# Performance work log

Measured on AMD Instinct MI355X. Metric: run time of the kernel, lower is better.

The kernel has to match this reference:

```python
import jax, jax.numpy as jnp
import numpy as np

SOFTCAP = 50.0
EPS = 1e-6
N_HEADS, D_HEAD = 16, 64


def _rms(x, w):
    return x * jax.lax.rsqrt(jnp.mean(x * x, axis=-1, keepdims=True) + EPS) * w


def _rope(x, cos, sin):
    # Faithful to source: apply_rope uses x.size(1) as the position axis, but is
    # called on (B, H, T, Dh) tensors, so positions are indexed by HEAD index.
    n = x.shape[1]
    x1, x2 = x[..., 0::2], x[..., 1::2]
    c = cos[:n][None, :, None, :]
    s = sin[:n][None, :, None, :]
    return jnp.stack([x1 * c - x2 * s, x1 * s + x2 * c], axis=-1).reshape(x.shape)


def setup_inputs() -> dict:
    key = jax.random.key(0)
    ks = jax.random.split(key, 12)
    L, D, H, Dh, Dff, V, B, T = 6, 1024, N_HEADS, D_HEAD, 4096, 32000, 1, 1024
    r = lambda k, shape: jax.random.normal(k, shape, dtype=jnp.float32) * 0.02
    return {
        'x': jax.random.randint(ks[0], (B, T), 0, V, dtype=jnp.int32),
        'embed': r(ks[1], (V, D)),
        'ln1': jnp.ones((L, D), jnp.float32),
        'Wq': r(ks[2], (L, H * Dh, D)),
        'Wk': r(ks[3], (L, H * Dh, D)),
        'Wv': r(ks[4], (L, H * Dh, D)),
        'Wo': r(ks[5], (L, D, H * Dh)),
        'qn': jnp.ones((L, Dh), jnp.float32),
        'kn': jnp.ones((L, Dh), jnp.float32),
        'ln2': jnp.ones((L, D), jnp.float32),
        'Wg': r(ks[6], (L, Dff, D)),
        'Wu': r(ks[7], (L, Dff, D)),
        'Wd': r(ks[8], (L, D, Dff)),
        'ln_out': jnp.ones((D,), jnp.float32),
    }


def reference(x, embed, ln1, Wq, Wk, Wv, Wo, qn, kn, ln2, Wg, Wu, Wd, ln_out):
    B, T = x.shape
    H, Dh = N_HEADS, D_HEAD
    scale = Dh ** -0.5
    # RoPE tables (theta=10000)
    freqs = 1.0 / (10000.0 ** (jnp.arange(0, Dh, 2, dtype=jnp.float32) / Dh))
    ang = jnp.arange(T, dtype=jnp.float32)[:, None] * freqs[None, :]
    cos, sin = jnp.cos(ang), jnp.sin(ang)
    mask = jnp.triu(jnp.ones((T, T), dtype=bool), k=1)  # True above diagonal

    h = embed[x]  # (B, T, D)

    def block(h, p):
        l1, wq, wk, wv, wo, qnw, knw, l2, wg, wu, wd = p
        hn = _rms(h, l1)
        q = (hn @ wq.T).reshape(B, T, H, Dh).transpose(0, 2, 1, 3)  # (B,H,T,Dh)
        k = (hn @ wk.T).reshape(B, T, H, Dh).transpose(0, 2, 1, 3)
        v = (hn @ wv.T).reshape(B, T, H, Dh).transpose(0, 2, 1, 3)
        q = _rope(_rms(q, qnw), cos, sin)
        k = _rope(_rms(k, knw), cos, sin)
        scores = jnp.einsum('bhtd,bhsd->bhts', q, k) * scale
        scores = SOFTCAP * jnp.tanh(scores / SOFTCAP)
        scores = jnp.where(mask[None, None], -jnp.inf, scores)
        attn = jax.nn.softmax(scores, axis=-1)
        o = jnp.einsum('bhts,bhsd->bhtd', attn, v)
        o = o.transpose(0, 2, 1, 3).reshape(B, T, H * Dh)
        h = h + o @ wo.T
        hn2 = _rms(h, l2)
        h = h + (jax.nn.silu(hn2 @ wg.T) * (hn2 @ wu.T)) @ wd.T
        return h, None

    h, _ = jax.lax.scan(block, h, (ln1, Wq, Wk, Wv, Wo, qn, kn, ln2, Wg, Wu, Wd))
    # tied embed/head
    logits = _rms(h, ln_out) @ embed.T  # (B, T, V)
    return logits
```

## Files before the change

kernel.cpp:

```cpp
#include <hip/hip_runtime.h>
#include <math.h>
#include <type_traits>

typedef __bf16 bf16_t;
typedef bf16_t bf16x4 __attribute__((ext_vector_type(4)));
typedef bf16_t bf16x8 __attribute__((ext_vector_type(8)));
typedef float  f32x4  __attribute__((ext_vector_type(4)));

#define RMS_EPS 1e-6f

enum { EP_STORE = 0, EP_RESID = 1, EP_SPLIT = 2, EP_SILU = 3, EP_QKV = 4 };

template<int V> using IC = std::integral_constant<int, V>;

static __device__ __forceinline__ f32x4 mfma16(bf16x8 a, bf16x8 b, f32x4 c) {
    return __builtin_amdgcn_mfma_f32_16x16x32_bf16(a, b, c, 0, 0, 0);
}

#define GLDS(gp, lp) __builtin_amdgcn_global_load_lds( \
    (const __attribute__((address_space(1))) void*)(gp), \
    (__attribute__((address_space(3))) void*)(lp), 16, 0, 0)

template<int N> static __device__ __forceinline__ void vmwait() {
    if constexpr (N == 0)      asm volatile("s_waitcnt vmcnt(0)" ::: "memory");
    else if constexpr (N == 2) asm volatile("s_waitcnt vmcnt(2)" ::: "memory");
    else if constexpr (N == 3) asm volatile("s_waitcnt vmcnt(3)" ::: "memory");
    else if constexpr (N == 4) asm volatile("s_waitcnt vmcnt(4)" ::: "memory");
    else if constexpr (N == 6) asm volatile("s_waitcnt vmcnt(6)" ::: "memory");
    else if constexpr (N == 8) asm volatile("s_waitcnt vmcnt(8)" ::: "memory");
    __builtin_amdgcn_sched_barrier(0);
}
static __device__ __forceinline__ void bar() { __builtin_amdgcn_s_barrier(); }

template<int BM, int BN, int WR, int WC, int PLANES, int EPIL, int MINW>
__global__ __launch_bounds__(WR * WC * 64, MINW)
void gemm_bf16(const bf16_t* __restrict__ Ah, const bf16_t* __restrict__ Al,
               const bf16_t* __restrict__ Bh,
               float* __restrict__ Cf, bf16_t* __restrict__ Ch, bf16_t* __restrict__ Cl,
               int K, int lda, int ldb, int ldc, long long sC,
               const float* __restrict__ qnw, const float* __restrict__ knw)
{
    constexpr int ASZ = BM * 32, BSZ = BN * 32;
    constexpr int NW = WR * WC;
    constexpr int NLD = (BM / 16 * (PLANES >= 2 ? 2 : 1) + BN / 16) / NW;
    __shared__ __align__(16) bf16_t sAh[2][ASZ], sBh[2][BSZ];
    __shared__ __align__(16) bf16_t sAl[PLANES >= 2 ? 2 : 1][PLANES >= 2 ? ASZ : 8];

    const int gx = gridDim.x;
    int id = blockIdx.x + gx * blockIdx.y;
    if (gridDim.z == 1) {
        int nwg = gx * gridDim.y;
        int q = nwg >> 3, r = nwg & 7;
        int xcd = id & 7, ix = id >> 3;
        id = (xcd < r ? xcd * (q + 1) : r * (q + 1) + (xcd - r) * q) + ix;
    }
    const int bm = id % gx, bn = id / gx;
    const int row0 = bm * BM, col0 = bn * BN;

    const size_t kofs = (size_t)blockIdx.z * K;
    Ah += kofs;  Bh += kofs;
    if constexpr (PLANES >= 2) Al += kofs;

    const int tid = threadIdx.x, lane = tid & 63, wave = tid >> 6;
    const int lr = lane & 15, lg = lane >> 4;
    constexpr int WM = BM / WR, WN = BN / WC, MF = WM / 16, NF = WN / 16;
    const int wr = wave / WC, wc = wave % WC;

    f32x4 acc[MF][NF];
    #pragma unroll
    for (int m = 0; m < MF; ++m)
        #pragma unroll
        for (int n = 0; n < NF; ++n) acc[m][n] = (f32x4){0.f, 0.f, 0.f, 0.f};

    auto stage = [&](int k0, auto pc) {
        constexpr int p = decltype(pc)::value;
        #pragma unroll
        for (int i = wave; i < BM / 16; i += NW) {
            int s = i * 64 + lane, rr = s >> 2, c = s & 3;
            size_t go = (size_t)(row0 + rr) * lda + k0 + ((c ^ ((rr >> 1) & 3)) << 3);
            GLDS(Ah + go, &sAh[p][i * 512]);
            if constexpr (PLANES >= 2) GLDS(Al + go, &sAl[p][i * 512]);
        }
        #pragma unroll
        for (int i = wave; i < BN / 16; i += NW) {
            int s = i * 64 + lane, rr = s >> 2, c = s & 3;
            size_t go = (size_t)(col0 + rr) * ldb + k0 + ((c ^ ((rr >> 1) & 3)) << 3);
            GLDS(Bh + go, &sBh[p][i * 512]);
        }
    };

    auto compute = [&](auto pc) {
        constexpr int p = decltype(pc)::value;
        bf16x8 ahf[MF], alf[MF], bhf[NF];
        #pragma unroll
        for (int m = 0; m < MF; ++m) {
            int rr = wr * WM + m * 16 + lr;
            int by = rr * 64 + ((lg ^ ((rr >> 1) & 3)) << 4);
            ahf[m] = *(const bf16x8*)((const char*)&sAh[p][0] + by);
            if constexpr (PLANES >= 2)
                alf[m] = *(const bf16x8*)((const char*)&sAl[p][0] + by);
        }
        #pragma unroll
        for (int n = 0; n < NF; ++n) {
            int rr = wc * WN + n * 16 + lr;
            int by = rr * 64 + ((lg ^ ((rr >> 1) & 3)) << 4);
            bhf[n] = *(const bf16x8*)((const char*)&sBh[p][0] + by);
        }
        #pragma unroll
        for (int m = 0; m < MF; ++m)
            #pragma unroll
            for (int n = 0; n < NF; ++n) {
                acc[m][n] = mfma16(ahf[m], bhf[n], acc[m][n]);
                if constexpr (PLANES >= 2)
                    acc[m][n] = mfma16(alf[m], bhf[n], acc[m][n]);
            }
    };

    stage(0, IC<0>{});
    int k0 = 32;
    for (; k0 + 32 < K; k0 += 64) {
        stage(k0, IC<1>{});
        vmwait<NLD>(); bar();
        compute(IC<0>{});
        bar();
        stage(k0 + 32, IC<0>{});
        vmwait<NLD>(); bar();
        compute(IC<1>{});
        bar();
    }
    stage(k0, IC<1>{});
    vmwait<NLD>(); bar();
    compute(IC<0>{});
    bar();
    vmwait<0>(); bar();
    compute(IC<1>{});

    if constexpr (EPIL == EP_QKV) {
        const int colbase = col0 + wc * WN;
        const int typ = colbase >> 10;
        const float* nw = (typ == 0) ? qnw : knw;
        const int hh = (colbase - typ * 1024) >> 6;
        constexpr float kLogF = -0.41524101186092029f;
        #pragma unroll
        for (int m = 0; m < MF; ++m)
            #pragma unroll
            for (int r = 0; r < 4; ++r) {
                int grow = row0 + wr * WM + m * 16 + lg * 4 + r;
                if (typ < 2) {
                    float ss = 0.f;
                    #pragma unroll
                    for (int n = 0; n < NF; ++n) {
                        float v = acc[m][n][r];
                        ss += v * v;
                    }
                    ss += __shfl_xor(ss, 1, 64);
                    ss += __shfl_xor(ss, 2, 64);
                    ss += __shfl_xor(ss, 4, 64);
                    ss += __shfl_xor(ss, 8, 64);
                    float inv = rsqrtf(ss * (1.0f / 64.0f) + RMS_EPS);
                    #pragma unroll
                    for (int n = 0; n < NF; ++n) {
                        int i = n * 16 + lr;
                        float x = acc[m][n][r] * inv * nw[i];
                        float p = __shfl_xor(x, 1, 64);
                        float f = exp2f((float)(i >> 1) * kLogF);
                        float ang = (float)hh * f;
                        float cs = cosf(ang), sn = sinf(ang);
                        float o = (lr & 1) ? (p * sn + x * cs) : (x * cs - p * sn);
                        Ch[(size_t)grow * ldc + colbase + i] = (bf16_t)o;
                    }
                } else {
                    #pragma unroll
                    for (int n = 0; n < NF; ++n) {
                        float v = acc[m][n][r];
                        size_t off = (size_t)grow * ldc + colbase + n * 16 + lr;
                        bf16_t hb = (bf16_t)v;
                        Ch[off] = hb;
                        Cl[off] = (bf16_t)(v - (float)hb);
                    }
                }
            }
        return;
    }

    #pragma unroll
    for (int m = 0; m < MF; ++m)
        #pragma unroll
        for (int n = 0; n < NF; ++n)
            #pragma unroll
            for (int r = 0; r < 4; ++r) {
                int grow = row0 + wr * WM + m * 16 + lg * 4 + r;
                int gcol = col0 + wc * WN + n * 16 + lr;
                float v = acc[m][n][r];
                if constexpr (EPIL == EP_SILU) {
                    float pv = __shfl_xor(v, 1, 64);
                    if (!(lr & 1)) {
                        float s = (v / (1.0f + expf(-v))) * pv;
                        size_t off = (size_t)grow * ldc + (gcol >> 1);
                        Ch[off] = (bf16_t)s;
                    }
                } else {
                    size_t off = (size_t)blockIdx.z * sC + (size_t)grow * ldc + gcol;
                    if constexpr (EPIL == EP_STORE) {
                        Cf[off] = v;
                    } else if constexpr (EPIL == EP_RESID) {
                        Cf[off] += v;
                    } else {
                        bf16_t hb = (bf16_t)v;
                        Ch[off] = hb;
                        Cl[off] = (bf16_t)(v - (float)hb);
                    }
                }
            }
}

static __device__ __forceinline__ void wsplit_body(
    int b2, int tid,
    const float* wq, const float* wk, const float* wv, const float* wo,
    const float* wg, const float* wu, const float* wd,
    bf16_t* wAh, bf16_t* wGUh, bf16_t* wdh)
{
    #pragma unroll
    for (int k = 0; k < 4; ++k) {
        int b = b2 * 4 + k;
        const float* src;
        bf16_t* dst;
        size_t so, doff;
        if (b < 4096) {
            src = b < 1024 ? wq : b < 2048 ? wk : b < 3072 ? wv : wo;
            so = (size_t)(b & 1023) * 256 + tid;
            doff = (size_t)b * 256 + tid;
            dst = wAh;
        } else if (b < 12288) {
            int bb = b - 4096;
            int row = bb < 4096 ? 2 * bb : 2 * (bb - 4096) + 1;
            src = bb < 4096 ? wg : wu;
            so = (size_t)(bb & 4095) * 256 + tid;
            doff = (size_t)row * 256 + tid;
            dst = wGUh;
        } else {
            src = wd;
            so = (size_t)(b - 12288) * 256 + tid;
            doff = so;
            dst = wdh;
        }
        f32x4 v = ((const f32x4*)src)[so];
        bf16x4 hv;
        #pragma unroll
        for (int j = 0; j < 4; ++j) hv[j] = (bf16_t)v[j];
        ((bf16x4*)dst)[doff] = hv;
    }
}

__global__ __launch_bounds__(256)
void reduce_rms_wsplit(const float* __restrict__ p, float* __restrict__ h,
                       const float* __restrict__ w, bf16_t* __restrict__ outh,
                       const float* wq, const float* wk, const float* wv,
                       const float* wo, const float* wg, const float* wu,
                       const float* wd, bf16_t* wAh, bf16_t* wGUh, bf16_t* wdh)
{
    int blk = blockIdx.x, tid = threadIdx.x;
    if (blk >= 1024) {
        if (wq) wsplit_body(blk - 1024, tid, wq, wk, wv, wo, wg, wu, wd,
                            wAh, wGUh, wdh);
        return;
    }
    size_t i = (size_t)blk * 256 + tid;
    const size_t S = (1024 * 1024) / 4;
    f32x4 a = ((const f32x4*)p)[i];
    f32x4 b = ((const f32x4*)p)[i + S];
    f32x4 c = ((const f32x4*)p)[i + 2 * S];
    f32x4 d = ((const f32x4*)p)[i + 3 * S];
    f32x4 hv = ((const f32x4*)h)[i];
    #pragma unroll
    for (int j = 0; j < 4; ++j) hv[j] += (a[j] + b[j]) + (c[j] + d[j]);
    ((f32x4*)h)[i] = hv;

    float ss = hv[0]*hv[0] + hv[1]*hv[1] + hv[2]*hv[2] + hv[3]*hv[3];
    #pragma unroll
    for (int m = 1; m < 64; m <<= 1) ss += __shfl_xor(ss, m, 64);
    __shared__ float red[4];
    if ((tid & 63) == 0) red[tid >> 6] = ss;
    __syncthreads();
    float tot = red[0] + red[1] + red[2] + red[3];
    float inv = rsqrtf(tot * (1.0f / 1024.0f) + RMS_EPS);
    f32x4 wt4 = *(const f32x4*)(w + tid * 4);
    bf16x4 hv4;
    #pragma unroll
    for (int j = 0; j < 4; ++j) hv4[j] = (bf16_t)(hv[j] * inv * wt4[j]);
    ((bf16x4*)outh)[i] = hv4;
}

__global__ __launch_bounds__(256)
void gather_rms_wsplit(const int* __restrict__ ids, const float* __restrict__ embed,
                       const float* __restrict__ w, float* __restrict__ h,
                       bf16_t* __restrict__ outh,
                       const float* wq, const float* wk, const float* wv,
                       const float* wo, const float* wg, const float* wu,
                       const float* wd, bf16_t* wAh, bf16_t* wGUh, bf16_t* wdh)
{
    int blk = blockIdx.x, tid = threadIdx.x;
    if (blk >= 1024) {
        wsplit_body(blk - 1024, tid, wq, wk, wv, wo, wg, wu, wd, wAh, wGUh, wdh);
        return;
    }
    int row = ids[blk];
    f32x4 v = ((const f32x4*)(embed + (size_t)row * 1024))[tid];
    ((f32x4*)(h + (size_t)blk * 1024))[tid] = v;

    float ss = v[0]*v[0] + v[1]*v[1] + v[2]*v[2] + v[3]*v[3];
    #pragma unroll
    for (int m = 1; m < 64; m <<= 1) ss += __shfl_xor(ss, m, 64);
    __shared__ float red[4];
    if ((tid & 63) == 0) red[tid >> 6] = ss;
    __syncthreads();
    float tot = red[0] + red[1] + red[2] + red[3];
    float inv = rsqrtf(tot * (1.0f / 1024.0f) + RMS_EPS);
    f32x4 wt4 = *(const f32x4*)(w + tid * 4);
    bf16x4 hv;
    #pragma unroll
    for (int j = 0; j < 4; ++j) hv[j] = (bf16_t)(v[j] * inv * wt4[j]);
    ((bf16x4*)outh)[(size_t)blk * 256 + tid] = hv;
}

__global__ __launch_bounds__(128, 2)
void flash_attn(const bf16_t* __restrict__ qkvh,
                const bf16_t* __restrict__ vTh, const bf16_t* __restrict__ vTl,
                bf16_t* __restrict__ oh)
{
    __shared__ __align__(16) bf16_t sQ[32*64], sK[64*64], sVh[64*64], sVl[64*64];
    __shared__ __align__(16) bf16_t sPh[32*64], sPl[32*64];

    const int q0 = blockIdx.x * 32;
    const int hh = blockIdx.y;
    const int tid = threadIdx.x, lane = tid & 63, w = tid >> 6;
    const int lr = lane & 15, lg = lane >> 4;

    #pragma unroll
    for (int ii = 0; ii < 2; ++ii) {
        int r0 = w * 16 + ii * 8;
        int r  = r0 + (lane >> 3);
        int i  = lane & 7;
        GLDS(qkvh + (size_t)(q0 + r) * 3072 + hh * 64 + ((i ^ (r & 7)) << 3),
             sQ + r0 * 64);
    }
    __syncthreads();

    bf16x8 qa[2];
    #pragma unroll
    for (int ks = 0; ks < 2; ++ks) {
        int r = w * 16 + lr;
        qa[ks] = *(const bf16x8*)((const char*)sQ + r * 128 +
                                  ((((ks << 2) | lg) ^ (r & 7)) << 4));
    }

    f32x4 o_acc[4];
    #pragma unroll
    for (int n = 0; n < 4; ++n) o_acc[n] = (f32x4){0.f, 0.f, 0.f, 0.f};
    float m_run[4] = {-1e30f, -1e30f, -1e30f, -1e30f};
    float l_run[4] = {0.f, 0.f, 0.f, 0.f};

    const int ntiles = ((q0 + 31) >> 6) + 1;
    for (int t = 0; t < ntiles; ++t) {
        const int kv0 = t * 64;
        #pragma unroll
        for (int ii = 0; ii < 4; ++ii) {
            int r0 = w * 32 + ii * 8;
            int r  = r0 + (lane >> 3);
            int i  = lane & 7;
            GLDS(qkvh + (size_t)(kv0 + r) * 3072 + 1024 + hh * 64 + ((i ^ (r & 7)) << 3),
                 sK + r0 * 64);
            GLDS(vTh + (size_t)(hh * 64 + r) * 1024 + kv0 + ((i ^ (r & 7)) << 3),
                 sVh + r0 * 64);
            GLDS(vTl + (size_t)(hh * 64 + r) * 1024 + kv0 + ((i ^ (r & 7)) << 3),
                 sVl + r0 * 64);
        }
        __syncthreads();

        f32x4 s_acc[4];
        #pragma unroll
        for (int n = 0; n < 4; ++n) s_acc[n] = (f32x4){0.f, 0.f, 0.f, 0.f};
        #pragma unroll
        for (int ks = 0; ks < 2; ++ks)
            #pragma unroll
            for (int n = 0; n < 4; ++n) {
                int r = n * 16 + lr;
                bf16x8 kb = *(const bf16x8*)((const char*)sK + r * 128 +
                                             ((((ks << 2) | lg) ^ (r & 7)) << 4));
                s_acc[n] = mfma16(qa[ks], kb, s_acc[n]);
            }

        #pragma unroll
        for (int j = 0; j < 4; ++j) {
            int qr = q0 + w * 16 + lg * 4 + j;
            float p[4];
            float mx = -1e30f;
            #pragma unroll
            for (int n = 0; n < 4; ++n) {
                float v = s_acc[n][j] * 0.125f;
                v = 50.f * tanhf(v * 0.02f);
                int key = kv0 + n * 16 + lr;
                if (key > qr) v = -1e30f;
                p[n] = v;
                mx = fmaxf(mx, v);
            }
            #pragma unroll
            for (int m = 1; m < 16; m <<= 1) mx = fmaxf(mx, __shfl_xor(mx, m, 64));
            float mn = fmaxf(m_run[j], mx);
            float ef = __expf(m_run[j] - mn);
            m_run[j] = mn;
            float rs = 0.f;
            #pragma unroll
            for (int n = 0; n < 4; ++n) {
                float e = expf(p[n] - mn);
                p[n] = e;
                rs += e;
            }
            #pragma unroll
            for (int m = 1; m < 16; m <<= 1) rs += __shfl_xor(rs, m, 64);
            l_run[j] = l_run[j] * ef + rs;
            #pragma unroll
            for (int n = 0; n < 4; ++n) o_acc[n][j] *= ef;
            int r = w * 16 + lg * 4 + j;
            #pragma unroll
            for (int n = 0; n < 4; ++n) {
                int c = n * 16 + lr;
                int byo = r * 128 + ((((c >> 3) ^ (r & 7)) << 4)) + ((c & 7) << 1);
                bf16_t hb = (bf16_t)p[n];
                *(bf16_t*)((char*)sPh + byo) = hb;
                *(bf16_t*)((char*)sPl + byo) = (bf16_t)(p[n] - (float)hb);
            }
        }

        #pragma unroll
        for (int ks = 0; ks < 2; ++ks) {
            int pr = w * 16 + lr;
            int pby = pr * 128 + ((((ks << 2) | lg) ^ (pr & 7)) << 4);
            bf16x8 pa  = *(const bf16x8*)((const char*)sPh + pby);
            bf16x8 pl_ = *(const bf16x8*)((const char*)sPl + pby);
            #pragma unroll
            for (int n = 0; n < 4; ++n) {
                int vr = n * 16 + lr;
                int vby = vr * 128 + ((((ks << 2) | lg) ^ (vr & 7)) << 4);
                bf16x8 vhf = *(const bf16x8*)((const char*)sVh + vby);
                bf16x8 vlf = *(const bf16x8*)((const char*)sVl + vby);
                o_acc[n] = mfma16(pa,  vhf, o_acc[n]);
                o_acc[n] = mfma16(pl_, vhf, o_acc[n]);
                o_acc[n] = mfma16(pa,  vlf, o_acc[n]);
            }
        }
        __syncthreads();
    }

    #pragma unroll
    for (int j = 0; j < 4; ++j) {
        float inv = 1.0f / l_run[j];
        int qr = q0 + w * 16 + lg * 4 + j;
        #pragma unroll
        for (int n = 0; n < 4; ++n) {
            size_t off = (size_t)qr * 1024 + hh * 64 + n * 16 + lr;
            oh[off] = (bf16_t)(o_acc[n][j] * inv);
        }
    }
}

__global__ __launch_bounds__(256)
void split_kernel(const float* __restrict__ src, bf16_t* __restrict__ hi)
{
    size_t i = (size_t)blockIdx.x * 256 + threadIdx.x;
    f32x4 v = ((const f32x4*)src)[i];
    bf16x4 hv;
    #pragma unroll
    for (int j = 0; j < 4; ++j) hv[j] = (bf16_t)v[j];
    ((bf16x4*)hi)[i] = hv;
}

__global__ __launch_bounds__(256)
void rmsnorm_split(const float* __restrict__ in, const float* __restrict__ w,
                   bf16_t* __restrict__ outh)
{
    int row = blockIdx.x, tid = threadIdx.x;
    f32x4 v = *(const f32x4*)(in + (size_t)row * 1024 + tid * 4);
    float ss = v[0]*v[0] + v[1]*v[1] + v[2]*v[2] + v[3]*v[3];
    #pragma unroll
    for (int m = 1; m < 64; m <<= 1) ss += __shfl_xor(ss, m, 64);
    __shared__ float red[4];
    if ((tid & 63) == 0) red[tid >> 6] = ss;
    __syncthreads();
    float tot = red[0] + red[1] + red[2] + red[3];
    float inv = rsqrtf(tot * (1.0f / 1024.0f) + RMS_EPS);
    f32x4 wt4 = *(const f32x4*)(w + tid * 4);
    bf16x4 hv;
    #pragma unroll
    for (int j = 0; j < 4; ++j) hv[j] = (bf16_t)(v[j] * inv * wt4[j]);
    ((bf16x4*)outh)[(size_t)row * 256 + tid] = hv;
}

__global__ __launch_bounds__(256)
void transpose_v(const bf16_t* __restrict__ qkvh, const bf16_t* __restrict__ qkvl,
                 bf16_t* __restrict__ vTh, bf16_t* __restrict__ vTl)
{
    __shared__ bf16_t tile[32][33];
    int b = blockIdx.x;
    int z = b >> 10, rem = b & 1023;
    const bf16_t* in = z ? qkvl : qkvh;
    bf16_t* out      = z ? vTl : vTh;
    int bx = (rem & 31) * 32, by = (rem >> 5) * 32;
    int r = threadIdx.x >> 5, c = threadIdx.x & 31;
    #pragma unroll
    for (int rr = r; rr < 32; rr += 8)
        tile[rr][c] = in[(size_t)(by + rr) * 3072 + 2048 + bx + c];
    __syncthreads();
    #pragma unroll
    for (int rr = r; rr < 32; rr += 8)
        out[(size_t)(bx + rr) * 1024 + by + c] = tile[c][rr];
}

extern "C" void kernel_launch(void* const* d_in, const int* in_sizes, int n_in,
                              void* d_out, int out_size, void* d_ws, size_t ws_size,
                              hipStream_t stream)
{
    (void)in_sizes; (void)n_in; (void)out_size; (void)ws_size;
    const int*   x_ids = (const int*)  d_in[0];
    const float* embed = (const float*)d_in[1];
    const float* ln1   = (const float*)d_in[2];
    const float* Wq    = (const float*)d_in[3];
    const float* Wk    = (const float*)d_in[4];
    const float* Wv    = (const float*)d_in[5];
    const float* Wo    = (const float*)d_in[6];
    const float* qn    = (const float*)d_in[7];
    const float* kn    = (const float*)d_in[8];
    const float* ln2   = (const float*)d_in[9];
    const float* Wg    = (const float*)d_in[10];
    const float* Wu    = (const float*)d_in[11];
    const float* Wd    = (const float*)d_in[12];
    const float* lnout = (const float*)d_in[13];
    float* out = (float*)d_out;

    char* ws = (char*)d_ws;
    const size_t MB = 1 << 20;
    float*  h    = (float*) (ws +   0 * MB);
    bf16_t* hnh  = (bf16_t*)(ws +   4 * MB);
    bf16_t* qkvh = (bf16_t*)(ws +   8 * MB);
    bf16_t* qkvl = (bf16_t*)(ws +  14 * MB);
    bf16_t* vTh  = (bf16_t*)(ws +  20 * MB);
    bf16_t* vTl  = (bf16_t*)(ws +  22 * MB);
    bf16_t* oh   = (bf16_t*)(ws +  24 * MB);
    bf16_t* wAh  = (bf16_t*)(ws +  28 * MB);
    bf16_t* wGUh = (bf16_t*)(ws +  36 * MB);
    bf16_t* wdh  = (bf16_t*)(ws +  52 * MB);
    bf16_t* silh = (bf16_t*)(ws +  60 * MB);
    float*  wdp  = (float*) (ws +  68 * MB);
    bf16_t* eh   = (bf16_t*)(ws +  84 * MB);

    const long long M1 = 1024 * 1024;

    gather_rms_wsplit<<<5120, 256, 0, stream>>>(
        x_ids, embed, ln1, h, hnh,
        Wq, Wk, Wv, Wo, Wg, Wu, Wd, wAh, wGUh, wdh);

    for (int l = 0; l < 6; ++l) {
        gemm_bf16<64,128,2,2,1,EP_QKV,4><<<dim3(16,24),256,0,stream>>>(
            hnh, nullptr, wAh, nullptr, qkvh, qkvl, 1024, 1024, 1024, 3072, 0,
            qn + l * 64, kn + l * 64);

        transpose_v<<<2048, 256, 0, stream>>>(qkvh, qkvl, vTh, vTl);

        flash_attn<<<dim3(32,16), 128, 0, stream>>>(qkvh, vTh, vTl, oh);

        gemm_bf16<64,64,2,2,1,EP_RESID,4><<<dim3(16,16),256,0,stream>>>(
            oh, nullptr, wAh + 3 * M1, h, nullptr, nullptr, 1024, 1024, 1024, 1024, 0,
            nullptr, nullptr);

        rmsnorm_split<<<1024, 256, 0, stream>>>(h, ln2 + l * 1024, hnh);

        gemm_bf16<128,256,2,4,1,EP_SILU,4><<<dim3(8,32),512,0,stream>>>(
            hnh, nullptr, wGUh, nullptr, silh, nullptr, 1024, 1024, 1024, 4096, 0,
            nullptr, nullptr);

        gemm_bf16<128,128,2,2,1,EP_STORE,4><<<dim3(8,8,4),256,0,stream>>>(
            silh, nullptr, wdh, wdp, nullptr, nullptr, 1024, 4096, 4096, 1024, M1,
            nullptr, nullptr);

        const float* wnext = (l < 5) ? (ln1 + (l + 1) * 1024) : lnout;
        if (l < 5) {
            reduce_rms_wsplit<<<5120, 256, 0, stream>>>(
                wdp, h, wnext, hnh,
                Wq + (size_t)(l+1) * M1, Wk + (size_t)(l+1) * M1,
                Wv + (size_t)(l+1) * M1, Wo + (size_t)(l+1) * M1,
                Wg + (size_t)(l+1) * 4 * M1, Wu + (size_t)(l+1) * 4 * M1,
                Wd + (size_t)(l+1) * 4 * M1, wAh, wGUh, wdh);
        } else {
            reduce_rms_wsplit<<<1024, 256, 0, stream>>>(
                wdp, h, wnext, hnh,
                nullptr, nullptr, nullptr, nullptr, nullptr, nullptr, nullptr,
                wAh, wGUh, wdh);
        }
    }

    split_kernel<<<32000, 256, 0, stream>>>(embed, eh);
    gemm_bf16<256,256,2,4,1,EP_STORE,2><<<dim3(4,125),512,0,stream>>>(
        hnh, nullptr, eh, out, nullptr, nullptr, 1024, 1024, 1024, 32000, 0,
        nullptr, nullptr);
}
```

Measured before the change: 1.243 ms.

## Add triple-buffered LDS pipeline to GEMMs and use fast exp/tanh intrinsics

Adds a DEPTH template parameter to the bf16 GEMM so most layer GEMMs use a three-stage LDS ring buffer. This keeps two K-chunks of global loads in flight while computing, with one barrier pair per step instead of the ping-pong schedule. The buffer index becomes a runtime value (j%3), which can add address arithmetic. The change also swaps expf for __expf in the SiLU epilogue and the attention softmax, and replaces tanhf in the softcap with an exp-based formula, which slightly changes numerics.

New measurement: 1.176 ms. 5.4% less time.

```diff
diff --git a/kernel.cpp b/kernel.cpp
--- a/kernel.cpp
+++ b/kernel.cpp
@@ -10,8 +10,6 @@
 #define RMS_EPS 1e-6f
 
 enum { EP_STORE = 0, EP_RESID = 1, EP_SPLIT = 2, EP_SILU = 3, EP_QKV = 4 };
-
-template<int V> using IC = std::integral_constant<int, V>;
 
 static __device__ __forceinline__ f32x4 mfma16(bf16x8 a, bf16x8 b, f32x4 c) {
     return __builtin_amdgcn_mfma_f32_16x16x32_bf16(a, b, c, 0, 0, 0);
@@ -32,7 +30,7 @@
 }
 static __device__ __forceinline__ void bar() { __builtin_amdgcn_s_barrier(); }
 
-template<int BM, int BN, int WR, int WC, int PLANES, int EPIL, int MINW>
+template<int BM, int BN, int WR, int WC, int PLANES, int EPIL, int MINW, int DEPTH>
 __global__ __launch_bounds__(WR * WC * 64, MINW)
 void gemm_bf16(const bf16_t* __restrict__ Ah, const bf16_t* __restrict__ Al,
                const bf16_t* __restrict__ Bh,
@@ -43,8 +41,8 @@
     constexpr int ASZ = BM * 32, BSZ = BN * 32;
     constexpr int NW = WR * WC;
     constexpr int NLD = (BM / 16 * (PLANES >= 2 ? 2 : 1) + BN / 16) / NW;
-    __shared__ __align__(16) bf16_t sAh[2][ASZ], sBh[2][BSZ];
-    __shared__ __align__(16) bf16_t sAl[PLANES >= 2 ? 2 : 1][PLANES >= 2 ? ASZ : 8];
+    __shared__ __align__(16) bf16_t sAh[DEPTH][ASZ], sBh[DEPTH][BSZ];
+    __shared__ __align__(16) bf16_t sAl[PLANES >= 2 ? DEPTH : 1][PLANES >= 2 ? ASZ : 8];
 
     const int gx = gridDim.x;
     int id = blockIdx.x + gx * blockIdx.y;
@@ -72,8 +70,7 @@
         #pragma unroll
         for (int n = 0; n < NF; ++n) acc[m][n] = (f32x4){0.f, 0.f, 0.f, 0.f};
 
-    auto stage = [&](int k0, auto pc) {
-        constexpr int p = decltype(pc)::value;
+    auto stage = [&](int k0, int p) {
         #pragma unroll
         for (int i = wave; i < BM / 16; i += NW) {
             int s = i * 64 + lane, rr = s >> 2, c = s & 3;
@@ -89,8 +86,7 @@
         }
     };
 
-    auto compute = [&](auto pc) {
-        constexpr int p = decltype(pc)::value;
+    auto compute = [&](int p) {
         bf16x8 ahf[MF], alf[MF], bhf[NF];
         #pragma unroll
         for (int m = 0; m < MF; ++m) {
@@ -116,24 +112,40 @@
             }
     };
 
-    stage(0, IC<0>{});
-    int k0 = 32;
-    for (; k0 + 32 < K; k0 += 64) {
-        stage(k0, IC<1>{});
+    if constexpr (DEPTH == 3) {
+        const int NC = K >> 5;
+        stage(0, 0);
+        stage(32, 1);
+        for (int j = 0; j + 2 < NC; ++j) {
+            stage(32 * (j + 2), (j + 2) % 3);
+            vmwait<2 * NLD>(); bar();
+            compute(j % 3);
+            bar();
+        }
         vmwait<NLD>(); bar();
-        compute(IC<0>{});
+        compute((K >> 5) >= 2 ? ((K >> 5) - 2) % 3 : 0);
+        vmwait<0>(); bar();
+        compute(((K >> 5) - 1) % 3);
+    } else {
+        stage(0, 0);
+        int k0 = 32;
+        for (; k0 + 32 < K; k0 += 64) {
+            stage(k0, 1);
+            vmwait<NLD>(); bar();
+            compute(0);
+            bar();
+            stage(k0 + 32, 0);
+            vmwait<NLD>(); bar();
+            compute(1);
+            bar();
+        }
+        stage(k0, 1);
+        vmwait<NLD>(); bar();
+        compute(0);
         bar();
-        stage(k0 + 32, IC<0>{});
-        vmwait<NLD>(); bar();
-        compute(IC<1>{});
-        bar();
-    }
-    stage(k0, IC<1>{});
-    vmwait<NLD>(); bar();
-    compute(IC<0>{});
-    bar();
-    vmwait<0>(); bar();
-    compute(IC<1>{});
+        vmwait<0>(); bar();
+        compute(1);
+    }
 
     if constexpr (EPIL == EP_QKV) {
         const int colbase = col0 + wc * WN;
@@ -195,7 +207,7 @@
                 if constexpr (EPIL == EP_SILU) {
                     float pv = __shfl_xor(v, 1, 64);
                     if (!(lr & 1)) {
-                        float s = (v / (1.0f + expf(-v))) * pv;
+                        float s = (v / (1.0f + __expf(-v))) * pv;
                         size_t off = (size_t)grow * ldc + (gcol >> 1);
                         Ch[off] = (bf16_t)s;
                     }
@@ -397,8 +409,8 @@
             float mx = -1e30f;
             #pragma unroll
             for (int n = 0; n < 4; ++n) {
-                float v = s_acc[n][j] * 0.125f;
-                v = 50.f * tanhf(v * 0.02f);
+                float sx = s_acc[n][j] * (0.125f * 0.02f);
+                float v = 50.f * (1.f - 2.f / (1.f + __expf(2.f * sx)));
                 int key = kv0 + n * 16 + lr;
                 if (key > qr) v = -1e30f;
                 p[n] = v;
@@ -412,7 +424,7 @@
             float rs = 0.f;
             #pragma unroll
             for (int n = 0; n < 4; ++n) {
-                float e = expf(p[n] - mn);
+                float e = __expf(p[n] - mn);
                 p[n] = e;
                 rs += e;
             }
@@ -560,7 +572,7 @@
         Wq, Wk, Wv, Wo, Wg, Wu, Wd, wAh, wGUh, wdh);
 
     for (int l = 0; l < 6; ++l) {
-        gemm_bf16<64,128,2,2,1,EP_QKV,4><<<dim3(16,24),256,0,stream>>>(
+        gemm_bf16<64,128,2,2,1,EP_QKV,4,3><<<dim3(16,24),256,0,stream>>>(
             hnh, nullptr, wAh, nullptr, qkvh, qkvl, 1024, 1024, 1024, 3072, 0,
             qn + l * 64, kn + l * 64);
 
@@ -568,17 +580,17 @@
 
         flash_attn<<<dim3(32,16), 128, 0, stream>>>(qkvh, vTh, vTl, oh);
 
-        gemm_bf16<64,64,2,2,1,EP_RESID,4><<<dim3(16,16),256,0,stream>>>(
+        gemm_bf16<64,64,2,2,1,EP_RESID,4,3><<<dim3(16,16),256,0,stream>>>(
             oh, nullptr, wAh + 3 * M1, h, nullptr, nullptr, 1024, 1024, 1024, 1024, 0,
             nullptr, nullptr);
 
         rmsnorm_split<<<1024, 256, 0, stream>>>(h, ln2 + l * 1024, hnh);
 
-        gemm_bf16<128,256,2,4,1,EP_SILU,4><<<dim3(8,32),512,0,stream>>>(
+        gemm_bf16<128,256,2,4,1,EP_SILU,4,3><<<dim3(8,32),512,0,stream>>>(
             hnh, nullptr, wGUh, nullptr, silh, nullptr, 1024, 1024, 1024, 4096, 0,
             nullptr, nullptr);
 
-        gemm_bf16<128,128,2,2,1,EP_STORE,4><<<dim3(8,8,4),256,0,stream>>>(
+        gemm_bf16<128,128,2,2,1,EP_STORE,4,3><<<dim3(8,8,4),256,0,stream>>>(
             silh, nullptr, wdh, wdp, nullptr, nullptr, 1024, 4096, 4096, 1024, M1,
             nullptr, nullptr);
 
@@ -599,7 +611,7 @@
     }
 
     split_kernel<<<32000, 256, 0, stream>>>(embed, eh);
-    gemm_bf16<256,256,2,4,1,EP_STORE,2><<<dim3(4,125),512,0,stream>>>(
+    gemm_bf16<256,256,2,4,1,EP_STORE,2,2><<<dim3(4,125),512,0,stream>>>(
         hnh, nullptr, eh, out, nullptr, nullptr, 1024, 1024, 1024, 32000, 0,
         nullptr, nullptr);
 }
```
